# Kernel optimization log

Hardware: AMD Instinct MI355X
Metric: run time of the kernel (lower is better)

## Reference

```python
import jax, jax.numpy as jnp
import numpy as np

B, T, E, H = 4, 1024, 2048, 32
D = E // H
BITS = 8


def fake_quant(x, axis=-1, bits=BITS):
    # dynamic asymmetric fake quantization (find_params + quantize + dequantize)
    maxq = float(2 ** bits - 1)
    xmax = jnp.maximum(jnp.max(x, axis=axis, keepdims=True), 0.0)
    xmin = jnp.minimum(jnp.min(x, axis=axis, keepdims=True), 0.0)
    scale = (xmax - xmin) / maxq
    scale = jnp.where(scale <= 0.0, 1.0, scale)
    zero = jnp.round(-xmin / scale)
    q = jnp.clip(jnp.round(x / scale) + zero, 0.0, maxq)
    return scale * (q - zero)


def setup_inputs() -> dict:
    key = jax.random.key(0)
    ks = jax.random.split(key, 9)
    std = 0.02
    hidden_states = jax.random.normal(ks[0], (B, T, E), jnp.float32)
    wq = jax.random.normal(ks[1], (E, E), jnp.float32) * std
    wk = jax.random.normal(ks[2], (E, E), jnp.float32) * std
    wv = jax.random.normal(ks[3], (E, E), jnp.float32) * std
    wo = jax.random.normal(ks[4], (E, E), jnp.float32) * std
    bq = jax.random.normal(ks[5], (E,), jnp.float32) * std
    bk = jax.random.normal(ks[6], (E,), jnp.float32) * std
    bv = jax.random.normal(ks[7], (E,), jnp.float32) * std
    bo = jax.random.normal(ks[8], (E,), jnp.float32) * std
    causal = jnp.tril(jnp.ones((T, T), dtype=bool))
    attention_mask = jnp.where(causal, 0.0, -1e9).astype(jnp.float32)[None, None]  # [1,1,T,T]
    return dict(hidden_states=hidden_states, wq=wq, bq=bq, wk=wk, bk=bk,
                wv=wv, bv=bv, wo=wo, bo=bo, attention_mask=attention_mask)


def reference(hidden_states, wq, bq, wk, bk, wv, bv, wo, bo, attention_mask):
    b, t, e = hidden_states.shape
    h, d = H, e // H
    scaling = d ** -0.5

    def split_heads(x):
        return x.reshape(b, t, h, d).transpose(0, 2, 1, 3)  # [b,h,t,d]

    q = split_heads((hidden_states @ wq.T + bq) * scaling)
    k = split_heads(hidden_states @ wk.T + bk)
    v = split_heads(hidden_states @ wv.T + bv)

    # SmoothK per_channel: divide K by per-channel (over tokens) abs-max, quantize
    # in the smoothed domain, rescale back.
    s = jnp.clip(jnp.max(jnp.abs(k), axis=2, keepdims=True), 1e-5, None)  # [b,h,1,d]
    k = fake_quant(k / s, axis=-1) * s

    q = fake_quant(q, axis=-1)           # per-token quant of Q
    v = fake_quant(v, axis=2)            # V quantized along sequence (transpose(2,3) path)

    attn = jnp.einsum('bhqd,bhkd->bhqk', q, k) + attention_mask
    probs = jax.nn.softmax(attn.astype(jnp.float32), axis=-1).astype(q.dtype)
    # dropout p=0 (eval); attn-weight quantization happens after probs are taken,
    # so it does not affect attn_output.
    out = jnp.einsum('bhqk,bhkd->bhqd', probs, v)
    out = out.transpose(0, 2, 1, 3).reshape(b, t, e)
    return out @ wo.T + bo
```

## Files before the change

kernel.cpp:

```cpp
#include <hip/hip_runtime.h>
#include <hip/hip_bf16.h>

typedef __hip_bfloat16 bf16;
typedef __attribute__((ext_vector_type(4))) short short4v;
typedef __attribute__((ext_vector_type(8))) short short8;
typedef __attribute__((ext_vector_type(4))) float f32x4;

#define NB 4
#define NT 1024
#define NE 2048
#define NH 32
#define ND 64
#define NBH (NB*NH)

__device__ __forceinline__ short bf16bits(float x) {
    bf16 h = __float2bfloat16(x);
    return *reinterpret_cast<short*>(&h);
}
__device__ __forceinline__ float bitsbf16(short s) {
    bf16 h = *reinterpret_cast<bf16*>(&s);
    return __bfloat162float(h);
}

__device__ __forceinline__ void gll16(const bf16* g, bf16* l) {
    __builtin_amdgcn_global_load_lds(
        (const __attribute__((address_space(1))) unsigned int*)g,
        (__attribute__((address_space(3))) unsigned int*)l, 16, 0, 0);
}

__global__ void detect_dtype(const unsigned short* __restrict__ w, int* __restrict__ flag) {
    int l = threadIdx.x;
    int big = 0;
    for (int i = l; i < 512; i += 64) {
        unsigned e = (w[i] >> 7) & 0xFFu;
        if (e >= 0x88u) big = 1;
    }
    unsigned long long m = __ballot(big != 0);
    if (l == 0) *flag = (m != 0ULL) ? 1 : 0;
}

__global__ __launch_bounds__(256) void conv_bf16(
    const void* __restrict__ src, bf16* __restrict__ dst, const int* __restrict__ flagp)
{
    const bool f32 = (*flagp != 0);
    size_t i = ((size_t)blockIdx.x * 256 + threadIdx.x) * 8;
    if (f32) {
        const float* s = (const float*)src + i;
        f32x4 a = *(const f32x4*)s;
        f32x4 b = *(const f32x4*)(s + 4);
        short8 r;
        r[0] = bf16bits(a[0]); r[1] = bf16bits(a[1]);
        r[2] = bf16bits(a[2]); r[3] = bf16bits(a[3]);
        r[4] = bf16bits(b[0]); r[5] = bf16bits(b[1]);
        r[6] = bf16bits(b[2]); r[7] = bf16bits(b[3]);
        *(short8*)(dst + i) = r;
    } else {
        *(short8*)(dst + i) = *(const short8*)((const bf16*)src + i);
    }
}

template<int MODE, int FUSE>
__global__ __launch_bounds__(256) void gemm_bf16(
    const bf16* __restrict__ A, const bf16* __restrict__ W,
    const void* __restrict__ bias, float scale, void* __restrict__ out,
    const int* __restrict__ flagp, int* __restrict__ st0, int* __restrict__ st1)
{
    const int K = NE, N = NE;
    __shared__ __align__(16) bf16 As[128 * 32];
    __shared__ __align__(16) bf16 Ws[128 * 32];
    int tid = threadIdx.x;
    int w = tid >> 6, l = tid & 63;
    int lr = l & 15, quad = l >> 4;
    int mBase = blockIdx.y * 128, nBase = blockIdx.x * 128;
    int mw = (w >> 1) * 64, nw = (w & 1) * 64;
    f32x4 acc[4][4] = {};

    const bf16* Ag = A + (size_t)(mBase + w * 16 + (l >> 2)) * K + (l & 3) * 8;
    const bf16* Wg = W + (size_t)(nBase + w * 16 + (l >> 2)) * K + (l & 3) * 8;
    bf16* AsW = As + (w * 16) * 32;
    bf16* WsW = Ws + (w * 16) * 32;

    for (int k0 = 0; k0 < K; k0 += 32) {
        gll16(Ag + k0, AsW);
        gll16(Ag + (size_t)64 * K + k0, AsW + 64 * 32);
        gll16(Wg + k0, WsW);
        gll16(Wg + (size_t)64 * K + k0, WsW + 64 * 32);
        __syncthreads();
        short8 af[4], bfr[4];
        #pragma unroll
        for (int i = 0; i < 4; i++)
            af[i] = *(const short8*)(As + (mw + i * 16 + lr) * 32 + quad * 8);
        #pragma unroll
        for (int j = 0; j < 4; j++)
            bfr[j] = *(const short8*)(Ws + (nw + j * 16 + lr) * 32 + quad * 8);
        #pragma unroll
        for (int i = 0; i < 4; i++)
            #pragma unroll
            for (int j = 0; j < 4; j++)
                acc[i][j] = __builtin_amdgcn_mfma_f32_16x16x32_bf16(
                    af[i], bfr[j], acc[i][j], 0, 0, 0);
        __syncthreads();
    }

    const bool f32 = (*flagp != 0);
    float bv[4];
    #pragma unroll
    for (int j = 0; j < 4; j++) {
        int n = nBase + nw + j * 16 + lr;
        bv[j] = f32 ? ((const float*)bias)[n] : bitsbf16(((const short*)bias)[n]);
    }
    float colA[4] = {0.f, 0.f, 0.f, 0.f};
    float colB[4] = {0.f, 0.f, 0.f, 0.f};

    #pragma unroll
    for (int i = 0; i < 4; i++) {
        float v[4][4];
        #pragma unroll
        for (int j = 0; j < 4; j++)
            #pragma unroll
            for (int r = 0; r < 4; r++)
                v[j][r] = (acc[i][j][r] + bv[j]) * scale;

        if (FUSE == 1) {
            #pragma unroll
            for (int r = 0; r < 4; r++) {
                float mx = 0.f, mn = 0.f;
                #pragma unroll
                for (int j = 0; j < 4; j++) { mx = fmaxf(mx, v[j][r]); mn = fminf(mn, v[j][r]); }
                #pragma unroll
                for (int off = 1; off < 16; off <<= 1) {
                    mx = fmaxf(mx, __shfl_xor(mx, off));
                    mn = fminf(mn, __shfl_xor(mn, off));
                }
                float sc = (mx - mn) * (1.f / 255.f);
                if (sc <= 0.f) sc = 1.f;
                float z = rintf(-mn / sc);
                #pragma unroll
                for (int j = 0; j < 4; j++) {
                    float q = fminf(fmaxf(rintf(v[j][r] / sc) + z, 0.f), 255.f);
                    v[j][r] = sc * (q - z);
                }
            }
        }
        if (FUSE == 2) {
            #pragma unroll
            for (int j = 0; j < 4; j++)
                #pragma unroll
                for (int r = 0; r < 4; r++)
                    colA[j] = fmaxf(colA[j], fabsf(v[j][r]));
        }
        if (FUSE == 3) {
            #pragma unroll
            for (int j = 0; j < 4; j++)
                #pragma unroll
                for (int r = 0; r < 4; r++) {
                    colA[j] = fmaxf(colA[j], v[j][r]);
                    colB[j] = fmaxf(colB[j], -v[j][r]);
                }
        }

        #pragma unroll
        for (int j = 0; j < 4; j++) {
            int n = nBase + nw + j * 16 + lr;
            #pragma unroll
            for (int r = 0; r < 4; r++) {
                int m = mBase + mw + i * 16 + quad * 4 + r;
                float vv = v[j][r];
                if (MODE == 0) {
                    if (f32) ((float*)out)[(size_t)m * N + n] = vv;
                    else     ((bf16*)out)[(size_t)m * N + n] = (bf16)vv;
                } else {
                    int b = m >> 10, t = m & (NT - 1);
                    int h = n >> 6, d = n & (ND - 1);
                    if (MODE == 1)
                        ((bf16*)out)[(((size_t)(b * NH + h)) * NT + t) * ND + d] = (bf16)vv;
                    else
                        ((bf16*)out)[(((size_t)(b * NH + h)) * ND + d) * NT + t] = (bf16)vv;
                }
            }
        }
    }

    if (FUSE == 2 || FUSE == 3) {
        int b = mBase >> 10;
        #pragma unroll
        for (int j = 0; j < 4; j++) {
            float a = colA[j], c = colB[j];
            a = fmaxf(a, __shfl_xor(a, 16)); a = fmaxf(a, __shfl_xor(a, 32));
            if (FUSE == 3) { c = fmaxf(c, __shfl_xor(c, 16)); c = fmaxf(c, __shfl_xor(c, 32)); }
            if (quad == 0) {
                int n = nBase + nw + j * 16 + lr;
                int idx = (b * NH + (n >> 6)) * 64 + (n & 63);
                atomicMax(st0 + idx, __float_as_int(a));
                if (FUSE == 3) atomicMax(st1 + idx, __float_as_int(c));
            }
        }
    }
}

__global__ __launch_bounds__(256) void quant_k(
    bf16* __restrict__ Kb, const int* __restrict__ sKbits)
{
    int bh = blockIdx.y;
    int t = blockIdx.x * 4 + (threadIdx.x >> 6);
    int l = threadIdx.x & 63;
    size_t idx = ((size_t)bh * NT + t) * ND + l;
    float s = fmaxf(__int_as_float(sKbits[bh * 64 + l]), 1e-5f);
    float x = (float)Kb[idx] / s;
    float mx = fmaxf(x, 0.f), mn = fminf(x, 0.f);
    #pragma unroll
    for (int off = 1; off < 64; off <<= 1) {
        mx = fmaxf(mx, __shfl_xor(mx, off));
        mn = fminf(mn, __shfl_xor(mn, off));
    }
    float sc = (mx - mn) * (1.f / 255.f);
    if (sc <= 0.f) sc = 1.f;
    float z = rintf(-mn / sc);
    float q = fminf(fmaxf(rintf(x / sc) + z, 0.f), 255.f);
    Kb[idx] = (bf16)(s * (sc * (q - z)));
}

__global__ __launch_bounds__(256) void quant_v2(
    bf16* __restrict__ Vt, const int* __restrict__ vMax, const int* __restrict__ vNeg)
{
    int bh = blockIdx.y;
    int d = blockIdx.x * 8 + (threadIdx.x >> 5);
    int c = (threadIdx.x & 31) * 8;
    float mx = __int_as_float(vMax[bh * 64 + d]);
    float mn = -__int_as_float(vNeg[bh * 64 + d]);
    float sc = (mx - mn) * (1.f / 255.f);
    if (sc <= 0.f) sc = 1.f;
    float z = rintf(-mn / sc);
    bf16* row = Vt + ((size_t)bh * ND + d) * NT;
    for (int seg = 0; seg < 4; seg++) {
        int off = seg * 256 + c;
        short8 v8 = *(const short8*)(row + off);
        #pragma unroll
        for (int k = 0; k < 8; k++) {
            float f = bitsbf16(v8[k]);
            float q = fminf(fmaxf(rintf(f / sc) + z, 0.f), 255.f);
            v8[k] = bf16bits(sc * (q - z));
        }
        *(short8*)(row + off) = v8;
    }
}

__global__ __launch_bounds__(256) void attn2(
    const bf16* __restrict__ Q, const bf16* __restrict__ K,
    const bf16* __restrict__ Vt, bf16* __restrict__ O)
{
    int bh = blockIdx.y;
    int b = bh >> 5, h = bh & 31;
    int qb = (int)gridDim.x - 1 - (int)blockIdx.x;
    int qBase = qb * 64;
    int w = threadIdx.x >> 6, l = threadIdx.x & 63;
    int lr = l & 15, quad = l >> 4;
    int qRow = qBase + w * 16;

    __shared__ __align__(16) bf16 Ks[2][64 * 64];
    __shared__ __align__(16) bf16 Vs[2][64 * 64];
    __shared__ __align__(16) bf16 Psh[4][16 * 64];

    const bf16* Kbase = K + (size_t)bh * NT * ND;
    const bf16* Vbase = Vt + (size_t)bh * ND * NT;

    const bf16* Qp = Q + ((size_t)bh * NT + qRow + lr) * ND + quad * 8;
    short8 qf0 = *(const short8*)Qp;
    short8 qf1 = *(const short8*)(Qp + 32);

    f32x4 o[4] = {};
    float m_i[4], l_i[4];
    #pragma unroll
    for (int r = 0; r < 4; r++) { m_i[r] = -1e30f; l_i[r] = 0.f; }

    int nkt = qb + 1;
    int srow = w * 16 + (l >> 3);
    int scol = (l & 7) * 8;

    auto stage = [&](int kt, int bufi) {
        int kc0 = kt * 64;
        #pragma unroll
        for (int c = 0; c < 2; c++) {
            gll16(Kbase + (size_t)(kc0 + srow + c * 8) * ND + scol,
                  &Ks[bufi][(w * 16 + c * 8) * 64]);
            gll16(Vbase + (size_t)(srow + c * 8) * NT + kc0 + scol,
                  &Vs[bufi][(w * 16 + c * 8) * 64]);
        }
    };
    stage(0, 0);

    for (int kt = 0; kt < nkt; kt++) {
        __syncthreads();
        if (kt + 1 < nkt) stage(kt + 1, (kt + 1) & 1);
        const bf16* Kt = Ks[kt & 1];
        const bf16* Vv = Vs[kt & 1];
        int kc0 = kt * 64;

        f32x4 s[4] = {};
        #pragma unroll
        for (int nb = 0; nb < 4; nb++) {
            short8 b0 = *(const short8*)(Kt + (nb * 16 + lr) * 64 + quad * 8);
            short8 b1 = *(const short8*)(Kt + (nb * 16 + lr) * 64 + 32 + quad * 8);
            s[nb] = __builtin_amdgcn_mfma_f32_16x16x32_bf16(qf0, b0, s[nb], 0, 0, 0);
            s[nb] = __builtin_amdgcn_mfma_f32_16x16x32_bf16(qf1, b1, s[nb], 0, 0, 0);
        }

        int row0 = qRow + quad * 4;
        float rmax[4];
        #pragma unroll
        for (int r = 0; r < 4; r++) rmax[r] = -1e30f;
        #pragma unroll
        for (int nb = 0; nb < 4; nb++) {
            int col = kc0 + nb * 16 + lr;
            #pragma unroll
            for (int r = 0; r < 4; r++) {
                if (col > row0 + r) s[nb][r] = -1e30f;
                rmax[r] = fmaxf(rmax[r], s[nb][r]);
            }
        }
        #pragma unroll
        for (int off = 1; off < 16; off <<= 1)
            #pragma unroll
            for (int r = 0; r < 4; r++)
                rmax[r] = fmaxf(rmax[r], __shfl_xor(rmax[r], off));

        float alpha[4], rsum[4];
        #pragma unroll
        for (int r = 0; r < 4; r++) {
            float mn2 = fmaxf(m_i[r], rmax[r]);
            alpha[r] = __expf(m_i[r] - mn2);
            m_i[r] = mn2;
            rsum[r] = 0.f;
        }
        #pragma unroll
        for (int nb = 0; nb < 4; nb++)
            #pragma unroll
            for (int r = 0; r < 4; r++) {
                float pp = __expf(s[nb][r] - m_i[r]);
                rsum[r] += pp;
                Psh[w][(quad * 4 + r) * 64 + nb * 16 + lr] = (bf16)pp;
            }
        #pragma unroll
        for (int off = 1; off < 16; off <<= 1)
            #pragma unroll
            for (int r = 0; r < 4; r++)
                rsum[r] += __shfl_xor(rsum[r], off);
        #pragma unroll
        for (int r = 0; r < 4; r++) l_i[r] = l_i[r] * alpha[r] + rsum[r];
        #pragma unroll
        for (int f = 0; f < 4; f++)
            #pragma unroll
            for (int r = 0; r < 4; r++)
                o[f][r] *= alpha[r];

        __syncthreads();
        short8 p0 = *(const short8*)(&Psh[w][lr * 64 + quad * 8]);
        short8 p1 = *(const short8*)(&Psh[w][lr * 64 + 32 + quad * 8]);
        #pragma unroll
        for (int f = 0; f < 4; f++) {
            short8 v0 = *(const short8*)(Vv + (f * 16 + lr) * 64 + quad * 8);
            short8 v1 = *(const short8*)(Vv + (f * 16 + lr) * 64 + 32 + quad * 8);
            o[f] = __builtin_amdgcn_mfma_f32_16x16x32_bf16(p0, v0, o[f], 0, 0, 0);
            o[f] = __builtin_amdgcn_mfma_f32_16x16x32_bf16(p1, v1, o[f], 0, 0, 0);
        }
    }

    float inv[4];
    #pragma unroll
    for (int r = 0; r < 4; r++) inv[r] = 1.f / l_i[r];
    #pragma unroll
    for (int f = 0; f < 4; f++)
        #pragma unroll
        for (int r = 0; r < 4; r++) {
            int t = qRow + quad * 4 + r;
            int d = f * 16 + lr;
            O[((size_t)(b * NT + t)) * NE + h * ND + d] = (bf16)(o[f][r] * inv[r]);
        }
}

__device__ __forceinline__ short8 ldfrag(const void* base, size_t off, bool f32) {
    if (f32) {
        const float* p = (const float*)base + off;
        f32x4 a = *(const f32x4*)p;
        f32x4 b = *(const f32x4*)(p + 4);
        short8 r;
        r[0] = bf16bits(a[0]); r[1] = bf16bits(a[1]);
        r[2] = bf16bits(a[2]); r[3] = bf16bits(a[3]);
        r[4] = bf16bits(b[0]); r[5] = bf16bits(b[1]);
        r[6] = bf16bits(b[2]); r[7] = bf16bits(b[3]);
        return r;
    }
    return *(const short8*)((const bf16*)base + off);
}

__device__ __forceinline__ void stage_tile(const void* __restrict__ src, bool f32,
                                           int rowBase, int k0, bf16* dst, int tid)
{
    const int K = NE;
    if (f32) {
        int r = tid >> 3;
        int c = (tid & 7) * 4;
        const float* p = (const float*)src + (size_t)(rowBase + r) * K + k0 + c;
        bf16* d = dst + r * 32 + c;
        #pragma unroll
        for (int i = 0; i < 4; i++) {
            f32x4 v = *(const f32x4*)(p + (size_t)(i * 32) * K);
            short4v o;
            o[0] = bf16bits(v[0]); o[1] = bf16bits(v[1]);
            o[2] = bf16bits(v[2]); o[3] = bf16bits(v[3]);
            *(short4v*)(d + i * 32 * 32) = o;
        }
    } else {
        int r = tid >> 2;
        int c = (tid & 3) * 8;
        const bf16* p = (const bf16*)src + (size_t)(rowBase + r) * K + k0 + c;
        bf16* d = dst + r * 32 + c;
        #pragma unroll
        for (int i = 0; i < 2; i++)
            *(short8*)(d + i * 64 * 32) = *(const short8*)(p + (size_t)(i * 64) * K);
    }
}

template<bool A_DYN, int MODE>
__global__ __launch_bounds__(256) void gemm_bt(
    const void* __restrict__ A, const void* __restrict__ W,
    const void* __restrict__ bias, float scale, void* __restrict__ out,
    const int* __restrict__ flagp)
{
    const int K = NE, N = NE;
    const bool f32 = (*flagp != 0);
    __shared__ __align__(16) bf16 As[128 * 32];
    __shared__ __align__(16) bf16 Ws[128 * 32];
    int tid = threadIdx.x;
    int w = tid >> 6, l = tid & 63;
    int lr = l & 15, quad = l >> 4;
    int mBase = blockIdx.y * 128;
    int nBase = blockIdx.x * 128;
    int mw = (w >> 1) * 64, nw = (w & 1) * 64;
    f32x4 acc[4][4] = {};
    for (int k0 = 0; k0 < K; k0 += 32) {
        stage_tile(A, A_DYN && f32, mBase, k0, As, tid);
        stage_tile(W, f32, nBase, k0, Ws, tid);
        __syncthreads();
        short8 af[4], bfr[4];
        #pragma unroll
        for (int i = 0; i < 4; i++)
            af[i] = *(const short8*)(As + (mw + i * 16 + lr) * 32 + quad * 8);
        #pragma unroll
        for (int j = 0; j < 4; j++)
            bfr[j] = *(const short8*)(Ws + (nw + j * 16 + lr) * 32 + quad * 8);
        #pragma unroll
        for (int i = 0; i < 4; i++)
            #pragma unroll
            for (int j = 0; j < 4; j++)
                acc[i][j] = __builtin_amdgcn_mfma_f32_16x16x32_bf16(
                    af[i], bfr[j], acc[i][j], 0, 0, 0);
        __syncthreads();
    }
    #pragma unroll
    for (int i = 0; i < 4; i++) {
        #pragma unroll
        for (int j = 0; j < 4; j++) {
            int n = nBase + nw + j * 16 + lr;
            float bv = f32 ? ((const float*)bias)[n] : bitsbf16(((const short*)bias)[n]);
            #pragma unroll
            for (int r = 0; r < 4; r++) {
                int m = mBase + mw + i * 16 + quad * 4 + r;
                float v = (acc[i][j][r] + bv) * scale;
                if (MODE == 0) {
                    if (f32) ((float*)out)[(size_t)m * N + n] = v;
                    else     ((bf16*)out)[(size_t)m * N + n] = (bf16)v;
                } else {
                    int b = m >> 10, t = m & (NT - 1);
                    int h = n >> 6, d = n & (ND - 1);
                    if (MODE == 1)
                        ((bf16*)out)[(((size_t)(b * NH + h)) * NT + t) * ND + d] = (bf16)v;
                    else
                        ((bf16*)out)[(((size_t)(b * NH + h)) * ND + d) * NT + t] = (bf16)v;
                }
            }
        }
    }
}

__global__ __launch_bounds__(256) void stats_k(
    const bf16* __restrict__ K, float* __restrict__ sK)
{
    int bh = blockIdx.x;
    int d = threadIdx.x & 63, tg = threadIdx.x >> 6;
    const bf16* Kp = K + (size_t)bh * NT * ND;
    float kabs = 0.f;
    for (int t = tg; t < NT; t += 4)
        kabs = fmaxf(kabs, fabsf((float)Kp[t * ND + d]));
    __shared__ float sh[4][64];
    sh[tg][d] = kabs;
    __syncthreads();
    if (threadIdx.x < 64) {
        kabs = fmaxf(fmaxf(sh[0][d], sh[1][d]), fmaxf(sh[2][d], sh[3][d]));
        sK[bh * 64 + d] = fmaxf(kabs, 1e-5f);
    }
}

__global__ __launch_bounds__(256) void stats_v(
    const bf16* __restrict__ Vt, float* __restrict__ vScale, float* __restrict__ vZero)
{
    int bh = blockIdx.x;
    int c = threadIdx.x >> 2;
    int seg = threadIdx.x & 3;
    const bf16* row = Vt + ((size_t)bh * ND + c) * NT + seg * 256;
    float vmax = 0.f, vmin = 0.f;
    for (int i = 0; i < 256; i += 8) {
        short8 v8 = *(const short8*)(row + i);
        for (int j = 0; j < 8; j++) {
            float f = bitsbf16(v8[j]);
            vmax = fmaxf(vmax, f);
            vmin = fminf(vmin, f);
        }
    }
    vmax = fmaxf(vmax, __shfl_xor(vmax, 1));
    vmax = fmaxf(vmax, __shfl_xor(vmax, 2));
    vmin = fminf(vmin, __shfl_xor(vmin, 1));
    vmin = fminf(vmin, __shfl_xor(vmin, 2));
    if (seg == 0) {
        float sc = (vmax - vmin) * (1.f / 255.f);
        if (sc <= 0.f) sc = 1.f;
        vScale[bh * 64 + c] = sc;
        vZero[bh * 64 + c] = rintf(-vmin / sc);
    }
}

__global__ __launch_bounds__(256) void quant_qk(
    bf16* __restrict__ Q, bf16* __restrict__ K, const float* __restrict__ sK)
{
    int bh = blockIdx.y;
    int t = blockIdx.x * 4 + (threadIdx.x >> 6);
    int l = threadIdx.x & 63;
    size_t idx = ((size_t)bh * NT + t) * ND + l;
    {
        float x = (float)Q[idx];
        float xmax = fmaxf(x, 0.f), xmin = fminf(x, 0.f);
        for (int off = 1; off < 64; off <<= 1) {
            xmax = fmaxf(xmax, __shfl_xor(xmax, off));
            xmin = fminf(xmin, __shfl_xor(xmin, off));
        }
        float sc = (xmax - xmin) * (1.f / 255.f);
        if (sc <= 0.f) sc = 1.f;
        float z = rintf(-xmin / sc);
        float q = fminf(fmaxf(rintf(x / sc) + z, 0.f), 255.f);
        Q[idx] = (bf16)(sc * (q - z));
    }
    {
        float s = sK[bh * 64 + l];
        float x = (float)K[idx] / s;
        float xmax = fmaxf(x, 0.f), xmin = fminf(x, 0.f);
        for (int off = 1; off < 64; off <<= 1) {
            xmax = fmaxf(xmax, __shfl_xor(xmax, off));
            xmin = fminf(xmin, __shfl_xor(xmin, off));
        }
        float sc = (xmax - xmin) * (1.f / 255.f);
        if (sc <= 0.f) sc = 1.f;
        float z = rintf(-xmin / sc);
        float q = fminf(fmaxf(rintf(x / sc) + z, 0.f), 255.f);
        K[idx] = (bf16)(s * (sc * (q - z)));
    }
}

__global__ __launch_bounds__(256) void quant_v_old(
    bf16* __restrict__ Vt,
    const float* __restrict__ vScale, const float* __restrict__ vZero)
{
    int bh = blockIdx.y, d = blockIdx.x;
    float sc = vScale[bh * 64 + d], z = vZero[bh * 64 + d];
    bf16* row = Vt + ((size_t)bh * ND + d) * NT;
    for (int t = threadIdx.x; t < NT; t += 256) {
        float v = (float)row[t];
        float q = fminf(fmaxf(rintf(v / sc) + z, 0.f), 255.f);
        row[t] = (bf16)(sc * (q - z));
    }
}

extern "C" void kernel_launch(void* const* d_in, const int* in_sizes, int n_in,
                              void* d_out, int out_size, void* d_ws, size_t ws_size,
                              hipStream_t stream)
{
    (void)in_sizes; (void)n_in; (void)out_size;
    const void* hs = d_in[0];
    const void* wq = d_in[1];
    const void* bq = d_in[2];
    const void* wk = d_in[3];
    const void* bk = d_in[4];
    const void* wv = d_in[5];
    const void* bv = d_in[6];
    const void* wo = d_in[7];
    const void* bo = d_in[8];

    const size_t qkvE = (size_t)NBH * NT * ND;
    const size_t qkvB = qkvE * 2;
    const size_t wBy  = (size_t)NE * NE * 2;
    const size_t statB = 3 * (size_t)NBH * ND * 4;
    const size_t needFast = 4 * qkvB + 4 * wBy + statB + 256;

    dim3 blk(256);
    dim3 gG(NE / 128, (NB * NT) / 128);
    const float scaling = 0.125f;

    if (ws_size >= needFast) {
        char* p = (char*)d_ws;
        bf16* Qb  = (bf16*)p; p += qkvB;
        bf16* Kb  = (bf16*)p; p += qkvB;
        bf16* Vt  = (bf16*)p; p += qkvB;
        bf16* hsB = (bf16*)p; p += qkvB;
        bf16* wqB = (bf16*)p; p += wBy;
        bf16* wkB = (bf16*)p; p += wBy;
        bf16* wvB = (bf16*)p; p += wBy;
        bf16* woB = (bf16*)p; p += wBy;
        int* sKb = (int*)p;
        int* vMx = sKb + NBH * ND;
        int* vNg = vMx + NBH * ND;
        int* flag = vNg + NBH * ND;
        bf16* Ab = hsB;

        detect_dtype<<<dim3(1), dim3(64), 0, stream>>>((const unsigned short*)wq, flag);
        hipMemsetAsync(sKb, 0, statB, stream);
        conv_bf16<<<dim3(4096), blk, 0, stream>>>(hs, hsB, flag);
        conv_bf16<<<dim3(2048), blk, 0, stream>>>(wq, wqB, flag);
        conv_bf16<<<dim3(2048), blk, 0, stream>>>(wk, wkB, flag);
        conv_bf16<<<dim3(2048), blk, 0, stream>>>(wv, wvB, flag);
        conv_bf16<<<dim3(2048), blk, 0, stream>>>(wo, woB, flag);
        gemm_bf16<1, 1><<<gG, blk, 0, stream>>>(hsB, wqB, bq, scaling, Qb, flag, nullptr, nullptr);
        gemm_bf16<1, 2><<<gG, blk, 0, stream>>>(hsB, wkB, bk, 1.0f, Kb, flag, sKb, nullptr);
        gemm_bf16<2, 3><<<gG, blk, 0, stream>>>(hsB, wvB, bv, 1.0f, Vt, flag, vMx, vNg);
        quant_k<<<dim3(NT / 4, NBH), blk, 0, stream>>>(Kb, sKb);
        quant_v2<<<dim3(ND / 8, NBH), blk, 0, stream>>>(Vt, vMx, vNg);
        attn2<<<dim3(NT / 64, NBH), blk, 0, stream>>>(Qb, Kb, Vt, Ab);
        gemm_bf16<0, 0><<<gG, blk, 0, stream>>>(Ab, woB, bo, 1.0f, d_out, flag, nullptr, nullptr);
    } else {
        bf16* Qb = (bf16*)d_ws;
        bf16* Kb = Qb + qkvE;
        bf16* Vt = Kb + qkvE;
        bf16* Ab = Vt + qkvE;
        float* sK  = (float*)(Ab + qkvE);
        float* vSc = sK + NBH * ND;
        float* vZp = vSc + NBH * ND;
        int*   flag = (int*)(vZp + NBH * ND);

        detect_dtype<<<dim3(1), dim3(64), 0, stream>>>((const unsigned short*)wq, flag);
        gemm_bt<true, 1><<<gG, blk, 0, stream>>>(hs, wq, bq, scaling, Qb, flag);
        gemm_bt<true, 1><<<gG, blk, 0, stream>>>(hs, wk, bk, 1.0f, Kb, flag);
        gemm_bt<true, 2><<<gG, blk, 0, stream>>>(hs, wv, bv, 1.0f, Vt, flag);
        stats_k<<<dim3(NBH), blk, 0, stream>>>(Kb, sK);
        stats_v<<<dim3(NBH), blk, 0, stream>>>(Vt, vSc, vZp);
        quant_qk<<<dim3(NT / 4, NBH), blk, 0, stream>>>(Qb, Kb, sK);
        quant_v_old<<<dim3(ND, NBH), blk, 0, stream>>>(Vt, vSc, vZp);
        attn2<<<dim3(NT / 64, NBH), blk, 0, stream>>>(Qb, Kb, Vt, Ab);
        gemm_bt<false, 0><<<gG, blk, 0, stream>>>(Ab, wo, bo, 1.0f, d_out, flag);
    }
}
```

Before: 536.8 us.

## Merge launches for conversion, QKV GEMM and quant; swizzle attention LDS

Folds the five dtype-conversion launches into one kernel and the three Q/K/V GEMMs into a single grid with z selecting the projection. The K and V quantization kernels are merged into one launch. The attention kernel gets an XOR swizzle on LDS rows for K, V and P to cut bank conflicts, and applies the causal mask only on the diagonal tile. This removes launch overhead and tail gaps between small kernels, at the cost of runtime branching on z in the GEMM epilogue and a hardcoded Q scaling of 0.125.

```diff
diff --git a/kernel.cpp b/kernel.cpp
--- a/kernel.cpp
+++ b/kernel.cpp
@@ -39,33 +39,51 @@
     if (l == 0) *flag = (m != 0ULL) ? 1 : 0;
 }
 
-__global__ __launch_bounds__(256) void conv_bf16(
-    const void* __restrict__ src, bf16* __restrict__ dst, const int* __restrict__ flagp)
+__global__ __launch_bounds__(256) void conv_all(
+    const void* __restrict__ hs, const void* __restrict__ wq, const void* __restrict__ wk,
+    const void* __restrict__ wv, const void* __restrict__ wo,
+    bf16* __restrict__ dhs, bf16* __restrict__ dwq, bf16* __restrict__ dwk,
+    bf16* __restrict__ dwv, bf16* __restrict__ dwo, const int* __restrict__ flagp)
 {
     const bool f32 = (*flagp != 0);
-    size_t i = ((size_t)blockIdx.x * 256 + threadIdx.x) * 8;
+    int bid = blockIdx.x;
+    const void* src; bf16* dst; size_t blk;
+    if (bid < 4096)      { src = hs; dst = dhs; blk = bid; }
+    else {
+        int r = (bid - 4096) >> 11, o = (bid - 4096) & 2047;
+        blk = o;
+        src = r == 0 ? wq : (r == 1 ? wk : (r == 2 ? wv : wo));
+        dst = r == 0 ? dwq : (r == 1 ? dwk : (r == 2 ? dwv : dwo));
+    }
+    size_t i = (blk * 256 + threadIdx.x) * 8;
     if (f32) {
         const float* s = (const float*)src + i;
         f32x4 a = *(const f32x4*)s;
         f32x4 b = *(const f32x4*)(s + 4);
-        short8 r;
-        r[0] = bf16bits(a[0]); r[1] = bf16bits(a[1]);
-        r[2] = bf16bits(a[2]); r[3] = bf16bits(a[3]);
-        r[4] = bf16bits(b[0]); r[5] = bf16bits(b[1]);
-        r[6] = bf16bits(b[2]); r[7] = bf16bits(b[3]);
-        *(short8*)(dst + i) = r;
+        short8 r8;
+        r8[0] = bf16bits(a[0]); r8[1] = bf16bits(a[1]);
+        r8[2] = bf16bits(a[2]); r8[3] = bf16bits(a[3]);
+        r8[4] = bf16bits(b[0]); r8[5] = bf16bits(b[1]);
+        r8[6] = bf16bits(b[2]); r8[7] = bf16bits(b[3]);
+        *(short8*)(dst + i) = r8;
     } else {
         *(short8*)(dst + i) = *(const short8*)((const bf16*)src + i);
     }
 }
 
-template<int MODE, int FUSE>
-__global__ __launch_bounds__(256) void gemm_bf16(
-    const bf16* __restrict__ A, const bf16* __restrict__ W,
-    const void* __restrict__ bias, float scale, void* __restrict__ out,
-    const int* __restrict__ flagp, int* __restrict__ st0, int* __restrict__ st1)
-{
-    const int K = NE, N = NE;
+__global__ __launch_bounds__(256) void gemm_qkv(
+    const bf16* __restrict__ A,
+    const bf16* __restrict__ Wq, const bf16* __restrict__ Wk, const bf16* __restrict__ Wv,
+    const void* __restrict__ bq, const void* __restrict__ bk, const void* __restrict__ bv,
+    bf16* __restrict__ Qb, bf16* __restrict__ Kb, bf16* __restrict__ Vt,
+    const int* __restrict__ flagp,
+    int* __restrict__ sKb, int* __restrict__ vMx, int* __restrict__ vNg)
+{
+    const int K = NE, z = blockIdx.z;
+    const bf16* W = z == 0 ? Wq : (z == 1 ? Wk : Wv);
+    const void* bias = z == 0 ? bq : (z == 1 ? bk : bv);
+    const float scale = z == 0 ? 0.125f : 1.0f;
+
     __shared__ __align__(16) bf16 As[128 * 32];
     __shared__ __align__(16) bf16 Ws[128 * 32];
     int tid = threadIdx.x;
@@ -103,11 +121,11 @@
     }
 
     const bool f32 = (*flagp != 0);
-    float bv[4];
+    float bv4[4];
     #pragma unroll
     for (int j = 0; j < 4; j++) {
         int n = nBase + nw + j * 16 + lr;
-        bv[j] = f32 ? ((const float*)bias)[n] : bitsbf16(((const short*)bias)[n]);
+        bv4[j] = f32 ? ((const float*)bias)[n] : bitsbf16(((const short*)bias)[n]);
     }
     float colA[4] = {0.f, 0.f, 0.f, 0.f};
     float colB[4] = {0.f, 0.f, 0.f, 0.f};
@@ -119,9 +137,9 @@
         for (int j = 0; j < 4; j++)
             #pragma unroll
             for (int r = 0; r < 4; r++)
-                v[j][r] = (acc[i][j][r] + bv[j]) * scale;
-
-        if (FUSE == 1) {
+                v[j][r] = (acc[i][j][r] + bv4[j]) * scale;
+
+        if (z == 0) {
             #pragma unroll
             for (int r = 0; r < 4; r++) {
                 float mx = 0.f, mn = 0.f;
@@ -134,22 +152,20 @@
                 }
                 float sc = (mx - mn) * (1.f / 255.f);
                 if (sc <= 0.f) sc = 1.f;
-                float z = rintf(-mn / sc);
+                float zq = rintf(-mn / sc);
                 #pragma unroll
                 for (int j = 0; j < 4; j++) {
-                    float q = fminf(fmaxf(rintf(v[j][r] / sc) + z, 0.f), 255.f);
-                    v[j][r] = sc * (q - z);
+                    float q = fminf(fmaxf(rintf(v[j][r] / sc) + zq, 0.f), 255.f);
+                    v[j][r] = sc * (q - zq);
                 }
             }
-        }
-        if (FUSE == 2) {
+        } else if (z == 1) {
             #pragma unroll
             for (int j = 0; j < 4; j++)
                 #pragma unroll
                 for (int r = 0; r < 4; r++)
                     colA[j] = fmaxf(colA[j], fabsf(v[j][r]));
-        }
-        if (FUSE == 3) {
+        } else {
             #pragma unroll
             for (int j = 0; j < 4; j++)
                 #pragma unroll
@@ -162,90 +178,143 @@
         #pragma unroll
         for (int j = 0; j < 4; j++) {
             int n = nBase + nw + j * 16 + lr;
+            int h = n >> 6, d = n & (ND - 1);
             #pragma unroll
             for (int r = 0; r < 4; r++) {
                 int m = mBase + mw + i * 16 + quad * 4 + r;
-                float vv = v[j][r];
-                if (MODE == 0) {
-                    if (f32) ((float*)out)[(size_t)m * N + n] = vv;
-                    else     ((bf16*)out)[(size_t)m * N + n] = (bf16)vv;
-                } else {
-                    int b = m >> 10, t = m & (NT - 1);
-                    int h = n >> 6, d = n & (ND - 1);
-                    if (MODE == 1)
-                        ((bf16*)out)[(((size_t)(b * NH + h)) * NT + t) * ND + d] = (bf16)vv;
-                    else
-                        ((bf16*)out)[(((size_t)(b * NH + h)) * ND + d) * NT + t] = (bf16)vv;
-                }
+                int b = m >> 10, t = m & (NT - 1);
+                if (z == 0)
+                    Qb[(((size_t)(b * NH + h)) * NT + t) * ND + d] = (bf16)v[j][r];
+                else if (z == 1)
+                    Kb[(((size_t)(b * NH + h)) * NT + t) * ND + d] = (bf16)v[j][r];
+                else
+                    Vt[(((size_t)(b * NH + h)) * ND + d) * NT + t] = (bf16)v[j][r];
             }
         }
     }
 
-    if (FUSE == 2 || FUSE == 3) {
+    if (z >= 1) {
         int b = mBase >> 10;
         #pragma unroll
         for (int j = 0; j < 4; j++) {
             float a = colA[j], c = colB[j];
             a = fmaxf(a, __shfl_xor(a, 16)); a = fmaxf(a, __shfl_xor(a, 32));
-            if (FUSE == 3) { c = fmaxf(c, __shfl_xor(c, 16)); c = fmaxf(c, __shfl_xor(c, 32)); }
+            if (z == 2) { c = fmaxf(c, __shfl_xor(c, 16)); c = fmaxf(c, __shfl_xor(c, 32)); }
             if (quad == 0) {
                 int n = nBase + nw + j * 16 + lr;
                 int idx = (b * NH + (n >> 6)) * 64 + (n & 63);
-                atomicMax(st0 + idx, __float_as_int(a));
-                if (FUSE == 3) atomicMax(st1 + idx, __float_as_int(c));
+                if (z == 1) atomicMax(sKb + idx, __float_as_int(a));
+                else { atomicMax(vMx + idx, __float_as_int(a)); atomicMax(vNg + idx, __float_as_int(c)); }
             }
         }
     }
 }
 
-__global__ __launch_bounds__(256) void quant_k(
-    bf16* __restrict__ Kb, const int* __restrict__ sKbits)
+__global__ __launch_bounds__(256) void gemm_o(
+    const bf16* __restrict__ A, const bf16* __restrict__ W,
+    const void* __restrict__ bias, void* __restrict__ out, const int* __restrict__ flagp)
+{
+    const int K = NE, N = NE;
+    __shared__ __align__(16) bf16 As[128 * 32];
+    __shared__ __align__(16) bf16 Ws[128 * 32];
+    int tid = threadIdx.x;
+    int w = tid >> 6, l = tid & 63;
+    int lr = l & 15, quad = l >> 4;
+    int mBase = blockIdx.y * 128, nBase = blockIdx.x * 128;
+    int mw = (w >> 1) * 64, nw = (w & 1) * 64;
+    f32x4 acc[4][4] = {};
+
+    const bf16* Ag = A + (size_t)(mBase + w * 16 + (l >> 2)) * K + (l & 3) * 8;
+    const bf16* Wg = W + (size_t)(nBase + w * 16 + (l >> 2)) * K + (l & 3) * 8;
+    bf16* AsW = As + (w * 16) * 32;
+    bf16* WsW = Ws + (w * 16) * 32;
+
+    for (int k0 = 0; k0 < K; k0 += 32) {
+        gll16(Ag + k0, AsW);
+        gll16(Ag + (size_t)64 * K + k0, AsW + 64 * 32);
+        gll16(Wg + k0, WsW);
+        gll16(Wg + (size_t)64 * K + k0, WsW + 64 * 32);
+        __syncthreads();
+        short8 af[4], bfr[4];
+        #pragma unroll
+        for (int i = 0; i < 4; i++)
+            af[i] = *(const short8*)(As + (mw + i * 16 + lr) * 32 + quad * 8);
+        #pragma unroll
+        for (int j = 0; j < 4; j++)
+            bfr[j] = *(const short8*)(Ws + (nw + j * 16 + lr) * 32 + quad * 8);
+        #pragma unroll
+        for (int i = 0; i < 4; i++)
+            #pragma unroll
+            for (int j = 0; j < 4; j++)
+                acc[i][j] = __builtin_amdgcn_mfma_f32_16x16x32_bf16(
+                    af[i], bfr[j], acc[i][j], 0, 0, 0);
+        __syncthreads();
+    }
+
+    const bool f32 = (*flagp != 0);
+    #pragma unroll
+    for (int i = 0; i < 4; i++) {
+        #pragma unroll
+        for (int j = 0; j < 4; j++) {
+            int n = nBase + nw + j * 16 + lr;
+            float bv = f32 ? ((const float*)bias)[n] : bitsbf16(((const short*)bias)[n]);
+            #pragma unroll
+            for (int r = 0; r < 4; r++) {
+                int m = mBase + mw + i * 16 + quad * 4 + r;
+                float vv = acc[i][j][r] + bv;
+                if (f32) ((float*)out)[(size_t)m * N + n] = vv;
+                else     ((bf16*)out)[(size_t)m * N + n] = (bf16)vv;
+            }
+        }
+    }
+}
+
+__global__ __launch_bounds__(256) void quant_kv(
+    bf16* __restrict__ Kb, bf16* __restrict__ Vt,
+    const int* __restrict__ sKbits, const int* __restrict__ vMax, const int* __restrict__ vNeg)
 {
     int bh = blockIdx.y;
-    int t = blockIdx.x * 4 + (threadIdx.x >> 6);
-    int l = threadIdx.x & 63;
-    size_t idx = ((size_t)bh * NT + t) * ND + l;
-    float s = fmaxf(__int_as_float(sKbits[bh * 64 + l]), 1e-5f);
-    float x = (float)Kb[idx] / s;
-    float mx = fmaxf(x, 0.f), mn = fminf(x, 0.f);
-    #pragma unroll
-    for (int off = 1; off < 64; off <<= 1) {
-        mx = fmaxf(mx, __shfl_xor(mx, off));
-        mn = fminf(mn, __shfl_xor(mn, off));
-    }
-    float sc = (mx - mn) * (1.f / 255.f);
-    if (sc <= 0.f) sc = 1.f;
-    float z = rintf(-mn / sc);
-    float q = fminf(fmaxf(rintf(x / sc) + z, 0.f), 255.f);
-    Kb[idx] = (bf16)(s * (sc * (q - z)));
-}
-
-__global__ __launch_bounds__(256) void quant_v2(
-    bf16* __restrict__ Vt, const int* __restrict__ vMax, const int* __restrict__ vNeg)
-{
-    int bh = blockIdx.y;
-    int d = blockIdx.x * 8 + (threadIdx.x >> 5);
-    int c = (threadIdx.x & 31) * 8;
-    float mx = __int_as_float(vMax[bh * 64 + d]);
-    float mn = -__int_as_float(vNeg[bh * 64 + d]);
-    float sc = (mx - mn) * (1.f / 255.f);
-    if (sc <= 0.f) sc = 1.f;
-    float z = rintf(-mn / sc);
-    bf16* row = Vt + ((size_t)bh * ND + d) * NT;
-    for (int seg = 0; seg < 4; seg++) {
-        int off = seg * 256 + c;
-        short8 v8 = *(const short8*)(row + off);
-        #pragma unroll
-        for (int k = 0; k < 8; k++) {
-            float f = bitsbf16(v8[k]);
-            float q = fminf(fmaxf(rintf(f / sc) + z, 0.f), 255.f);
-            v8[k] = bf16bits(sc * (q - z));
-        }
-        *(short8*)(row + off) = v8;
-    }
-}
-
-__global__ __launch_bounds__(256) void attn2(
+    if (blockIdx.x < 256) {
+        int t = blockIdx.x * 4 + (threadIdx.x >> 6);
+        int l = threadIdx.x & 63;
+        size_t idx = ((size_t)bh * NT + t) * ND + l;
+        float s = fmaxf(__int_as_float(sKbits[bh * 64 + l]), 1e-5f);
+        float x = (float)Kb[idx] / s;
+        float mx = fmaxf(x, 0.f), mn = fminf(x, 0.f);
+        #pragma unroll
+        for (int off = 1; off < 64; off <<= 1) {
+            mx = fmaxf(mx, __shfl_xor(mx, off));
+            mn = fminf(mn, __shfl_xor(mn, off));
+        }
+        float sc = (mx - mn) * (1.f / 255.f);
+        if (sc <= 0.f) sc = 1.f;
+        float z = rintf(-mn / sc);
+        float q = fminf(fmaxf(rintf(x / sc) + z, 0.f), 255.f);
+        Kb[idx] = (bf16)(s * (sc * (q - z)));
+    } else {
+        int d = (blockIdx.x - 256) * 8 + (threadIdx.x >> 5);
+        int c = (threadIdx.x & 31) * 8;
+        float mx = __int_as_float(vMax[bh * 64 + d]);
+        float mn = -__int_as_float(vNeg[bh * 64 + d]);
+        float sc = (mx - mn) * (1.f / 255.f);
+        if (sc <= 0.f) sc = 1.f;
+        float z = rintf(-mn / sc);
+        bf16* row = Vt + ((size_t)bh * ND + d) * NT;
+        for (int seg = 0; seg < 4; seg++) {
+            int off = seg * 256 + c;
+            short8 v8 = *(const short8*)(row + off);
+            #pragma unroll
+            for (int k = 0; k < 8; k++) {
+                float f = bitsbf16(v8[k]);
+                float q = fminf(fmaxf(rintf(f / sc) + z, 0.f), 255.f);
+                v8[k] = bf16bits(sc * (q - z));
+            }
+            *(short8*)(row + off) = v8;
+        }
+    }
+}
+
+__global__ __launch_bounds__(256) void attn3(
     const bf16* __restrict__ Q, const bf16* __restrict__ K,
     const bf16* __restrict__ Vt, bf16* __restrict__ O)
 {
@@ -275,7 +344,7 @@
 
     int nkt = qb + 1;
     int srow = w * 16 + (l >> 3);
-    int scol = (l & 7) * 8;
+    int scol = (((l & 7) ^ ((l >> 3) & 7))) * 8;
 
     auto stage = [&](int kt, int bufi) {
         int kc0 = kt * 64;
@@ -288,6 +357,9 @@
         }
     };
     stage(0, 0);
+
+    int slot0 = (quad ^ (lr & 7)) * 8;
+    int slot1 = ((quad ^ 4) ^ (lr & 7)) * 8;
 
     for (int kt = 0; kt < nkt; kt++) {
         __syncthreads();
@@ -299,8 +371,8 @@
         f32x4 s[4] = {};
         #pragma unroll
         for (int nb = 0; nb < 4; nb++) {
-            short8 b0 = *(const short8*)(Kt + (nb * 16 + lr) * 64 + quad * 8);
-            short8 b1 = *(const short8*)(Kt + (nb * 16 + lr) * 64 + 32 + quad * 8);
+            short8 b0 = *(const short8*)(Kt + (nb * 16 + lr) * 64 + slot0);
+            short8 b1 = *(const short8*)(Kt + (nb * 16 + lr) * 64 + slot1);
             s[nb] = __builtin_amdgcn_mfma_f32_16x16x32_bf16(qf0, b0, s[nb], 0, 0, 0);
             s[nb] = __builtin_amdgcn_mfma_f32_16x16x32_bf16(qf1, b1, s[nb], 0, 0, 0);
         }
@@ -309,14 +381,22 @@
         float rmax[4];
         #pragma unroll
         for (int r = 0; r < 4; r++) rmax[r] = -1e30f;
-        #pragma unroll
-        for (int nb = 0; nb < 4; nb++) {
-            int col = kc0 + nb * 16 + lr;
-            #pragma unroll
-            for (int r = 0; r < 4; r++) {
-                if (col > row0 + r) s[nb][r] = -1e30f;
-                rmax[r] = fmaxf(rmax[r], s[nb][r]);
+        if (kt == qb) {
+            #pragma unroll
+            for (int nb = 0; nb < 4; nb++) {
+                int col = kc0 + nb * 16 + lr;
+                #pragma unroll
+                for (int r = 0; r < 4; r++) {
+                    if (col > row0 + r) s[nb][r] = -1e30f;
+                    rmax[r] = fmaxf(rmax[r], s[nb][r]);
+                }
             }
+        } else {
+            #pragma unroll
+            for (int nb = 0; nb < 4; nb++)
+                #pragma unroll
+                for (int r = 0; r < 4; r++)
+                    rmax[r] = fmaxf(rmax[r], s[nb][r]);
         }
         #pragma unroll
         for (int off = 1; off < 16; off <<= 1)
@@ -333,13 +413,16 @@
             rsum[r] = 0.f;
         }
         #pragma unroll
-        for (int nb = 0; nb < 4; nb++)
+        for (int nb = 0; nb < 4; nb++) {
+            int cb = nb * 2 + (lr >> 3), ci = lr & 7;
             #pragma unroll
             for (int r = 0; r < 4; r++) {
                 float pp = __expf(s[nb][r] - m_i[r]);
                 rsum[r] += pp;
-                Psh[w][(quad * 4 + r) * 64 + nb * 16 + lr] = (bf16)pp;
+                int row = quad * 4 + r;
+                Psh[w][row * 64 + (cb ^ (row & 7)) * 8 + ci] = (bf16)pp;
             }
+        }
         #pragma unroll
         for (int off = 1; off < 16; off <<= 1)
             #pragma unroll
@@ -354,12 +437,12 @@
                 o[f][r] *= alpha[r];
 
         __syncthreads();
-        short8 p0 = *(const short8*)(&Psh[w][lr * 64 + quad * 8]);
-        short8 p1 = *(const short8*)(&Psh[w][lr * 64 + 32 + quad * 8]);
+        short8 p0 = *(const short8*)(&Psh[w][lr * 64 + slot0]);
+        short8 p1 = *(const short8*)(&Psh[w][lr * 64 + slot1]);
         #pragma unroll
         for (int f = 0; f < 4; f++) {
-            short8 v0 = *(const short8*)(Vv + (f * 16 + lr) * 64 + quad * 8);
-            short8 v1 = *(const short8*)(Vv + (f * 16 + lr) * 64 + 32 + quad * 8);
+            short8 v0 = *(const short8*)(Vv + (f * 16 + lr) * 64 + slot0);
+            short8 v1 = *(const short8*)(Vv + (f * 16 + lr) * 64 + slot1);
             o[f] = __builtin_amdgcn_mfma_f32_16x16x32_bf16(p0, v0, o[f], 0, 0, 0);
             o[f] = __builtin_amdgcn_mfma_f32_16x16x32_bf16(p1, v1, o[f], 0, 0, 0);
         }
@@ -376,21 +459,6 @@
             int d = f * 16 + lr;
             O[((size_t)(b * NT + t)) * NE + h * ND + d] = (bf16)(o[f][r] * inv[r]);
         }
-}
-
-__device__ __forceinline__ short8 ldfrag(const void* base, size_t off, bool f32) {
-    if (f32) {
-        const float* p = (const float*)base + off;
-        f32x4 a = *(const f32x4*)p;
-        f32x4 b = *(const f32x4*)(p + 4);
-        short8 r;
-        r[0] = bf16bits(a[0]); r[1] = bf16bits(a[1]);
-        r[2] = bf16bits(a[2]); r[3] = bf16bits(a[3]);
-        r[4] = bf16bits(b[0]); r[5] = bf16bits(b[1]);
-        r[6] = bf16bits(b[2]); r[7] = bf16bits(b[3]);
-        return r;
-    }
-    return *(const short8*)((const bf16*)base + off);
 }
 
 __device__ __forceinline__ void stage_tile(const void* __restrict__ src, bool f32,
@@ -622,18 +690,13 @@
 
         detect_dtype<<<dim3(1), dim3(64), 0, stream>>>((const unsigned short*)wq, flag);
         hipMemsetAsync(sKb, 0, statB, stream);
-        conv_bf16<<<dim3(4096), blk, 0, stream>>>(hs, hsB, flag);
-        conv_bf16<<<dim3(2048), blk, 0, stream>>>(wq, wqB, flag);
-        conv_bf16<<<dim3(2048), blk, 0, stream>>>(wk, wkB, flag);
-        conv_bf16<<<dim3(2048), blk, 0, stream>>>(wv, wvB, flag);
-        conv_bf16<<<dim3(2048), blk, 0, stream>>>(wo, woB, flag);
-        gemm_bf16<1, 1><<<gG, blk, 0, stream>>>(hsB, wqB, bq, scaling, Qb, flag, nullptr, nullptr);
-        gemm_bf16<1, 2><<<gG, blk, 0, stream>>>(hsB, wkB, bk, 1.0f, Kb, flag, sKb, nullptr);
-        gemm_bf16<2, 3><<<gG, blk, 0, stream>>>(hsB, wvB, bv, 1.0f, Vt, flag, vMx, vNg);
-        quant_k<<<dim3(NT / 4, NBH), blk, 0, stream>>>(Kb, sKb);
-        quant_v2<<<dim3(ND / 8, NBH), blk, 0, stream>>>(Vt, vMx, vNg);
-        attn2<<<dim3(NT / 64, NBH), blk, 0, stream>>>(Qb, Kb, Vt, Ab);
-        gemm_bf16<0, 0><<<gG, blk, 0, stream>>>(Ab, woB, bo, 1.0f, d_out, flag, nullptr, nullptr);
+        conv_all<<<dim3(4096 + 4 * 2048), blk, 0, stream>>>(
+            hs, wq, wk, wv, wo, hsB, wqB, wkB, wvB, woB, flag);
+        gemm_qkv<<<dim3(NE / 128, (NB * NT) / 128, 3), blk, 0, stream>>>(
+            hsB, wqB, wkB, wvB, bq, bk, bv, Qb, Kb, Vt, flag, sKb, vMx, vNg);
+        quant_kv<<<dim3(256 + ND / 8, NBH), blk, 0, stream>>>(Kb, Vt, sKb, vMx, vNg);
+        attn3<<<dim3(NT / 64, NBH), blk, 0, stream>>>(Qb, Kb, Vt, Ab);
+        gemm_o<<<gG, blk, 0, stream>>>(Ab, woB, bo, d_out, flag);
     } else {
         bf16* Qb = (bf16*)d_ws;
         bf16* Kb = Qb + qkvE;
@@ -652,7 +715,7 @@
         stats_v<<<dim3(NBH), blk, 0, stream>>>(Vt, vSc, vZp);
         quant_qk<<<dim3(NT / 4, NBH), blk, 0, stream>>>(Qb, Kb, sK);
         quant_v_old<<<dim3(ND, NBH), blk, 0, stream>>>(Vt, vSc, vZp);
-        attn2<<<dim3(NT / 64, NBH), blk, 0, stream>>>(Qb, Kb, Vt, Ab);
+        attn3<<<dim3(NT / 64, NBH), blk, 0, stream>>>(Qb, Kb, Vt, Ab);
         gemm_bt<false, 0><<<gG, blk, 0, stream>>>(Ab, wo, bo, 1.0f, d_out, flag);
     }
 }
```

Result: faster. 503.2 us (-6.2%).
